# Optimization experiments

Measured on AMD Instinct MI355X. Metric: run time of the kernel, lower is better.

## Reference

```python
import jax, jax.numpy as jnp
import numpy as np

T, L, N, DR = 8, 8, 500, 32
D = 2 * DR          # dr2 = 64
K = 12              # neighbors per region
S = 2               # number_sp attention layers


def setup_inputs() -> dict:
    key = jax.random.key(0)
    ks = jax.random.split(key, 14)
    inp = {}
    inp["all_data_static"] = jax.random.normal(ks[0], (T, L, N, D), jnp.float32)
    inp["thre_nc"] = jax.random.uniform(ks[1], (T, L, N, 1), jnp.float32)
    inp["all_data_dynamic_now"] = jax.random.uniform(ks[2], (L, N, D), jnp.float32)
    inp["neigh_poi"] = jax.random.randint(ks[3], (N, K), 0, N)
    inp["neigh_road"] = jax.random.randint(ks[4], (N, K), 0, N)
    inp["neigh_record"] = jax.random.randint(ks[5], (N, K), 0, N)
    inp["w1"] = jax.random.normal(ks[6], (2 * D, D), jnp.float32) * 0.05
    inp["wq_all"] = jax.random.normal(ks[7], (2, 3, S, D, D), jnp.float32) * 0.05
    inp["wk_all"] = jax.random.normal(ks[8], (2, 3, S, D, D), jnp.float32) * 0.05
    inp["wd_all"] = jax.random.normal(ks[9], (2, 3, S, D, D), jnp.float32) * 0.05
    inp["wmix_all"] = jax.random.normal(ks[10], (2, 3, D), jnp.float32) * 0.1
    inp["conv_w"] = jax.random.normal(ks[11], (4, 2 * D + 1), jnp.float32) * 0.05
    inp["conv_b"] = jnp.zeros((4,), jnp.float32)
    inp["fin_w"] = jax.random.normal(ks[12], (N, N), jnp.float32) * 0.02
    inp["fin_b"] = jnp.ones((N,), jnp.float32)
    return inp


def _attention(data, neigh, wq, wk, wd):
    # data: (T,L,N,D), neigh: (N,K)
    dn = data[:, :, neigh, :]                                   # (T,L,N,K,D) gather
    q = jnp.einsum('tlnd,de->tlne', data, wq)                   # (T,L,N,D)
    k = jnp.einsum('tlnkd,de->tlnke', dn, wk)                   # (T,L,N,K,D)
    a = jax.nn.softmax(jnp.einsum('tlne,tlnke->tlnk', q, k), -1)
    out = q + jnp.einsum('tlnk,tlnke->tlne', a, k)              # residual on q
    return jax.nn.sigmoid(jnp.einsum('tlnd,de->tlne', out, wd))


def _multiattention(data, neighs, wq, wk, wd, wmix):
    outs = []
    for g in range(3):  # poi, road, record
        x = data
        for s in range(wq.shape[1]):
            x = _attention(x, neighs[g], wq[g, s], wk[g, s], wd[g, s])
        outs.append(x)
    return jax.nn.sigmoid(outs[0] * wmix[0] + outs[1] * wmix[1] + outs[2] * wmix[2])


def reference(all_data_static, thre_nc, all_data_dynamic_now,
              neigh_poi, neigh_road, neigh_record,
              w1, wq_all, wk_all, wd_all, wmix_all,
              conv_w, conv_b, fin_w, fin_b):
    # --- Evolution: gated recurrence over time steps 1..T-1 ---
    def evo_step(now, xs):
        st, th = xs  # (L,N,D), (L,N,1)
        new = jax.nn.sigmoid(jnp.concatenate([now, st], -1) @ w1 * th
                             + now * (1.0 - th))
        return new, (new, new - now)
    now_final, (dyn_rest, diffs) = jax.lax.scan(
        evo_step, all_data_dynamic_now, (all_data_static[1:], thre_nc[1:]))
    all_dyn = jnp.concatenate([all_data_dynamic_now[None], dyn_rest], 0)  # (T,L,N,D)

    neighs = (neigh_poi, neigh_road, neigh_record)
    dyn = _multiattention(all_dyn, neighs, wq_all[0], wk_all[0], wd_all[0], wmix_all[0])
    sta = _multiattention(all_data_static, neighs, wq_all[1], wk_all[1], wd_all[1], wmix_all[1])
    x = jnp.concatenate([dyn, sta], -1)                          # (T,L,N,2D)

    # --- ConvLSTM, kernel (1,1), hidden_dim=1 -> pointwise gated recurrence ---
    h0 = jnp.zeros((x.shape[0], x.shape[2], 1), x.dtype)         # (T,N,1)
    def cell(carry, xt):  # xt: (T,N,2D)
        h, c = carry
        gates = jnp.concatenate([xt, h], -1) @ conv_w.T + conv_b  # (T,N,4)
        i = jax.nn.sigmoid(gates[..., 0:1])
        f = jax.nn.sigmoid(gates[..., 1:2])
        o = jax.nn.sigmoid(gates[..., 2:3])
        g = jnp.tanh(gates[..., 3:4])
        c2 = f * c + i * g
        h2 = o * jnp.tanh(c2)
        return (h2, c2), None
    (h_last, _), _ = jax.lax.scan(cell, (h0, h0), jnp.swapaxes(x, 0, 1))

    out = jax.nn.sigmoid(h_last[..., 0] @ fin_w.T + fin_b)       # (T,N)
    return out, now_final, diffs
```

## Files before the change

### kernel.cpp

```cpp
#include <hip/hip_runtime.h>
#include <math.h>

namespace {
constexpr int kT = 8, kL = 8, kN = 500, kD = 64, kK = 12;
constexpr int kLN  = kL * kN;
constexpr int kTLN = kT * kL * kN;
constexpr int kBUF = kTLN * kD;
constexpr int XS = 68;
constexpr int EVR = 16;
}

__device__ __forceinline__ float sigf(float v) { return 1.f / (1.f + __expf(-v)); }

__device__ __forceinline__ float tanh_fast(float v) {
    float e = __expf(-2.f * fabsf(v));
    float t = (1.f - e) / (1.f + e);
    return copysignf(t, v);
}

__device__ __forceinline__ float row_allreduce16(float v) {
    v += __int_as_float(__builtin_amdgcn_update_dpp(
            0, __float_as_int(v), 0xB1, 0xf, 0xf, true));
    v += __int_as_float(__builtin_amdgcn_update_dpp(
            0, __float_as_int(v), 0x4E, 0xf, 0xf, true));
    v += __int_as_float(__builtin_amdgcn_update_dpp(
            0, __float_as_int(v), 0x124, 0xf, 0xf, true));
    v += __int_as_float(__builtin_amdgcn_update_dpp(
            0, __float_as_int(v), 0x128, 0xf, 0xf, true));
    return v;
}

__device__ __forceinline__ void stage_x(const float* __restrict__ src, float* lds,
                                        int row0, int M) {
    int r  = threadIdx.x >> 4;
    int c4 = (threadIdx.x & 15) << 2;
#pragma unroll
    for (int i = 0; i < 4; ++i) {
        int rr  = r + 16 * i;
        int row = row0 + rr;
        row = row < M ? row : M - 1;
        float4 v = *reinterpret_cast<const float4*>(src + (size_t)row * 64 + c4);
        *reinterpret_cast<float4*>(lds + rr * XS + c4) = v;
    }
}

template <int K>
__device__ __forceinline__ void stage_w(const float* __restrict__ w, float* lds) {
    const float4* s = reinterpret_cast<const float4*>(w);
    float4* d = reinterpret_cast<float4*>(lds);
#pragma unroll
    for (int i = 0; i < K / 16; ++i)
        d[threadIdx.x + 256 * i] = s[threadIdx.x + 256 * i];
}

__device__ __forceinline__ void gemm_core_gw(const float* ldsx,
                                             const float* __restrict__ gw,
                                             int rblk, int cblk, float4 acc[4]) {
#pragma unroll 4
    for (int k = 0; k < 64; k += 4) {
        float4 xv[4], wv[4];
#pragma unroll
        for (int i = 0; i < 4; ++i)
            xv[i] = *reinterpret_cast<const float4*>(ldsx + (4 * rblk + i) * XS + k);
#pragma unroll
        for (int d = 0; d < 4; ++d)
            wv[d] = *reinterpret_cast<const float4*>(gw + (k + d) * 64 + 4 * cblk);
#pragma unroll
        for (int i = 0; i < 4; ++i) {
            float xs[4] = {xv[i].x, xv[i].y, xv[i].z, xv[i].w};
#pragma unroll
            for (int d = 0; d < 4; ++d) {
                acc[i].x = fmaf(xs[d], wv[d].x, acc[i].x);
                acc[i].y = fmaf(xs[d], wv[d].y, acc[i].y);
                acc[i].z = fmaf(xs[d], wv[d].z, acc[i].z);
                acc[i].w = fmaf(xs[d], wv[d].w, acc[i].w);
            }
        }
    }
}

__device__ __forceinline__ void gemm_core2_bal(const float* ldsx, const float* ldswa,
                                               const float* __restrict__ gwb,
                                               int rblk, int cblk,
                                               float4 acca[4], float4 accb[4]) {
#pragma unroll 4
    for (int k = 0; k < 64; k += 4) {
        float4 xv[4], wa[4], wb[4];
#pragma unroll
        for (int i = 0; i < 4; ++i)
            xv[i] = *reinterpret_cast<const float4*>(ldsx + (4 * rblk + i) * XS + k);
#pragma unroll
        for (int d = 0; d < 4; ++d) {
            wa[d] = *reinterpret_cast<const float4*>(ldswa + (k + d) * 64 + 4 * cblk);
            wb[d] = *reinterpret_cast<const float4*>(gwb + (k + d) * 64 + 4 * cblk);
        }
#pragma unroll
        for (int i = 0; i < 4; ++i) {
            float xs[4] = {xv[i].x, xv[i].y, xv[i].z, xv[i].w};
#pragma unroll
            for (int d = 0; d < 4; ++d) {
                acca[i].x = fmaf(xs[d], wa[d].x, acca[i].x);
                acca[i].y = fmaf(xs[d], wa[d].y, acca[i].y);
                acca[i].z = fmaf(xs[d], wa[d].z, acca[i].z);
                acca[i].w = fmaf(xs[d], wa[d].w, acca[i].w);
                accb[i].x = fmaf(xs[d], wb[d].x, accb[i].x);
                accb[i].y = fmaf(xs[d], wb[d].y, accb[i].y);
                accb[i].z = fmaf(xs[d], wb[d].z, accb[i].z);
                accb[i].w = fmaf(xs[d], wb[d].w, accb[i].w);
            }
        }
    }
}

__global__ void __launch_bounds__(256) evo_all_kernel(const float* __restrict__ stat,
                                                      const float* __restrict__ thre,
                                                      const float* __restrict__ dyn0,
                                                      float* __restrict__ all_dyn,
                                                      float* __restrict__ diff,
                                                      float* __restrict__ now_final,
                                                      const float* __restrict__ w1) {
    __shared__ float ldsn[EVR * XS];
    __shared__ float ldss[EVR * XS];
    __shared__ float ldsw[128 * 64];
    int row0 = blockIdx.x * EVR;
    int r  = threadIdx.x >> 4;
    int c4 = (threadIdx.x & 15) << 2;
    *reinterpret_cast<float4*>(ldsn + r * XS + c4) =
        *reinterpret_cast<const float4*>(dyn0 + (size_t)(row0 + r) * 64 + c4);
    stage_w<128>(w1, ldsw);
    __syncthreads();
    {
        float4 x0 = *reinterpret_cast<const float4*>(ldsn + r * XS + c4);
        *reinterpret_cast<float4*>(all_dyn + (size_t)(row0 + r) * 64 + c4) = x0;
    }
#pragma unroll 1
    for (int t = 1; t < kT; ++t) {
        *reinterpret_cast<float4*>(ldss + r * XS + c4) =
            *reinterpret_cast<const float4*>(stat + (size_t)t * kLN * kD
                                             + (size_t)(row0 + r) * 64 + c4);
        __syncthreads();
        float4 acc = {0.f, 0.f, 0.f, 0.f};
#pragma unroll 4
        for (int k = 0; k < 64; k += 4) {
            float4 xv = *reinterpret_cast<const float4*>(ldsn + r * XS + k);
            float xs[4] = {xv.x, xv.y, xv.z, xv.w};
#pragma unroll
            for (int d = 0; d < 4; ++d) {
                float4 wv = *reinterpret_cast<const float4*>(ldsw + (k + d) * 64 + c4);
                acc.x = fmaf(xs[d], wv.x, acc.x);
                acc.y = fmaf(xs[d], wv.y, acc.y);
                acc.z = fmaf(xs[d], wv.z, acc.z);
                acc.w = fmaf(xs[d], wv.w, acc.w);
            }
        }
#pragma unroll 4
        for (int k = 0; k < 64; k += 4) {
            float4 xv = *reinterpret_cast<const float4*>(ldss + r * XS + k);
            float xs[4] = {xv.x, xv.y, xv.z, xv.w};
#pragma unroll
            for (int d = 0; d < 4; ++d) {
                float4 wv = *reinterpret_cast<const float4*>(ldsw + (64 + k + d) * 64 + c4);
                acc.x = fmaf(xs[d], wv.x, acc.x);
                acc.y = fmaf(xs[d], wv.y, acc.y);
                acc.z = fmaf(xs[d], wv.z, acc.z);
                acc.w = fmaf(xs[d], wv.w, acc.w);
            }
        }
        int row = row0 + r;
        float tt = thre[t * kLN + row];
        float4 xn = *reinterpret_cast<const float4*>(ldsn + r * XS + c4);
        float4 nv;
        nv.x = sigf(acc.x * tt + xn.x * (1.f - tt));
        nv.y = sigf(acc.y * tt + xn.y * (1.f - tt));
        nv.z = sigf(acc.z * tt + xn.z * (1.f - tt));
        nv.w = sigf(acc.w * tt + xn.w * (1.f - tt));
        float4 df;
        df.x = nv.x - xn.x; df.y = nv.y - xn.y;
        df.z = nv.z - xn.z; df.w = nv.w - xn.w;
        *reinterpret_cast<float4*>(all_dyn + ((size_t)t * kLN + row) * 64 + c4) = nv;
        *reinterpret_cast<float4*>(diff + ((size_t)(t - 1) * kLN + row) * 64 + c4) = df;
        if (t == kT - 1)
            *reinterpret_cast<float4*>(now_final + (size_t)row * 64 + c4) = nv;
        __syncthreads();
        *reinterpret_cast<float4*>(ldsn + r * XS + c4) = nv;
    }
}

__global__ void __launch_bounds__(256) gemm_qk(const float* __restrict__ Xdyn,
                                               const float* __restrict__ Xstat,
                                               const float* __restrict__ wq_all,
                                               const float* __restrict__ wk_all,
                                               float* __restrict__ b1,
                                               float* __restrict__ b2, int step) {
    __shared__ float ldsx[64 * XS];
    __shared__ float ldswq[64 * 64];
    int c = blockIdx.y;
    int m = c / 3;
    float* b1c = b1 + (size_t)c * kBUF;
    float* b2c = b2 + (size_t)c * kBUF;
    const float* X = step ? b1c : (m == 0 ? Xdyn : Xstat);
    size_t woff = (size_t)(c * 2 + step) * kD * kD;
    int row0 = blockIdx.x * 64;
    stage_x(X, ldsx, row0, kTLN);
    stage_w<64>(wq_all + woff, ldswq);
    __syncthreads();
    int rblk = threadIdx.x >> 4, cblk = threadIdx.x & 15;
    float4 aq[4] = {}, ak[4] = {};
    gemm_core2_bal(ldsx, ldswq, wk_all + woff, rblk, cblk, aq, ak);
#pragma unroll
    for (int i = 0; i < 4; ++i) {
        size_t row = row0 + 4 * rblk + i;
        *reinterpret_cast<float4*>(b1c + row * 64 + 4 * cblk) = aq[i];
        *reinterpret_cast<float4*>(b2c + row * 64 + 4 * cblk) = ak[i];
    }
}

__global__ void __launch_bounds__(256) scorewd_kernel(float* __restrict__ b1,
                                                      const float* __restrict__ b2,
                                                      const int* __restrict__ npoi,
                                                      const int* __restrict__ nroad,
                                                      const int* __restrict__ nrec,
                                                      const float* __restrict__ wd_all,
                                                      int step) {
    __shared__ float ldsx[64 * XS];
    int p   = blockIdx.y * gridDim.x + blockIdx.x;
    int xcd = p & 7;
    int gid = xcd * 375 + (p >> 3);
    int c    = gid / 500;
    int tile = gid - c * 500;
    int g = c % 3;
    float* b1c = b1 + (size_t)c * kBUF;
    const float* b2c = b2 + (size_t)c * kBUF;
    const int* neigh = (g == 0) ? npoi : (g == 1) ? nroad : nrec;
    const float* gw = wd_all + (size_t)(c * 2 + step) * kD * kD;

    int lane = threadIdx.x & 63;
    int wv   = threadIdx.x >> 6;
    int sub  = lane >> 4;
    int gq   = lane & 15;
    int row0 = tile * 64;
#pragma unroll 1
    for (int pp = 0; pp < 4; ++pp) {
        int lr  = pp * 16 + wv * 4 + sub;
        int row = row0 + lr;
        int n   = row % kN;
        int slab = row - n;
        float4 q = *(reinterpret_cast<const float4*>(b1c) + (size_t)row * 16 + gq);
        const int4* nbp = reinterpret_cast<const int4*>(neigh + n * kK);
        int4 nb0 = nbp[0], nb1 = nbp[1], nb2 = nbp[2];
        int nb[12] = {nb0.x, nb0.y, nb0.z, nb0.w, nb1.x, nb1.y, nb1.z, nb1.w,
                      nb2.x, nb2.y, nb2.z, nb2.w};
        float4 kv[12];
        float sc[12];
#pragma unroll
        for (int j = 0; j < 12; ++j) {
            kv[j] = *(reinterpret_cast<const float4*>(b2c) + (size_t)(slab + nb[j]) * 16 + gq);
            sc[j] = q.x * kv[j].x + q.y * kv[j].y + q.z * kv[j].z + q.w * kv[j].w;
        }
#pragma unroll
        for (int j = 0; j < 12; ++j) sc[j] = row_allreduce16(sc[j]);
        float mx = sc[0];
#pragma unroll
        for (int j = 1; j < 12; ++j) mx = fmaxf(mx, sc[j]);
        float ssum = 0.f;
#pragma unroll
        for (int j = 0; j < 12; ++j) { sc[j] = __expf(sc[j] - mx); ssum += sc[j]; }
        float inv = 1.f / ssum;
        float4 o = q;
#pragma unroll
        for (int j = 0; j < 12; ++j) {
            float a = sc[j] * inv;
            o.x = fmaf(a, kv[j].x, o.x);
            o.y = fmaf(a, kv[j].y, o.y);
            o.z = fmaf(a, kv[j].z, o.z);
            o.w = fmaf(a, kv[j].w, o.w);
        }
        *reinterpret_cast<float4*>(ldsx + lr * XS + 4 * gq) = o;
    }
    __syncthreads();
    int rblk = threadIdx.x >> 4, cblk = threadIdx.x & 15;
    float4 acc[4] = {};
    gemm_core_gw(ldsx, gw, rblk, cblk, acc);
#pragma unroll
    for (int i = 0; i < 4; ++i) {
        size_t idx = ((size_t)(row0 + 4 * rblk + i)) * 64 + 4 * cblk;
        float4 y;
        y.x = sigf(acc[i].x); y.y = sigf(acc[i].y);
        y.z = sigf(acc[i].z); y.w = sigf(acc[i].w);
        *reinterpret_cast<float4*>(b1c + idx) = y;
    }
}

__global__ void __launch_bounds__(256) lstm_kernel(const float* __restrict__ b1,
                                                   const float* __restrict__ wmix,
                                                   const float* __restrict__ cw,
                                                   const float* __restrict__ cb,
                                                   float* __restrict__ hlast) {
    int lane = threadIdx.x & 63;
    int wv   = threadIdx.x >> 6;
    int sub  = lane >> 4;
    int fq   = lane & 15;
    int cell = blockIdx.x * 16 + wv * 4 + sub;
    int t = cell / kN, n = cell % kN;
    float wd_[4][4], ws_[4][4], wh[4], bb[4];
#pragma unroll
    for (int gg = 0; gg < 4; ++gg) {
#pragma unroll
        for (int k = 0; k < 4; ++k) {
            wd_[gg][k] = cw[gg * 129 + fq * 4 + k];
            ws_[gg][k] = cw[gg * 129 + 64 + fq * 4 + k];
        }
        wh[gg] = cw[gg * 129 + 128];
        bb[gg] = cb[gg];
    }
    float4 wm[6];
#pragma unroll
    for (int j = 0; j < 6; ++j)
        wm[j] = *reinterpret_cast<const float4*>(wmix + j * 64 + fq * 4);
    float h = 0.f, cc = 0.f;
#pragma unroll 1
    for (int l = 0; l < kL; ++l) {
        size_t row16 = ((size_t)(t * kL + l) * kN + n) * 16 + fq;
        float4 y[6];
#pragma unroll
        for (int j = 0; j < 6; ++j)
            y[j] = *(reinterpret_cast<const float4*>(b1) + (size_t)j * (kBUF / 4) + row16);
        float4 xd, xs;
        xd.x = sigf(y[0].x * wm[0].x + y[1].x * wm[1].x + y[2].x * wm[2].x);
        xd.y = sigf(y[0].y * wm[0].y + y[1].y * wm[1].y + y[2].y * wm[2].y);
        xd.z = sigf(y[0].z * wm[0].z + y[1].z * wm[1].z + y[2].z * wm[2].z);
        xd.w = sigf(y[0].w * wm[0].w + y[1].w * wm[1].w + y[2].w * wm[2].w);
        xs.x = sigf(y[3].x * wm[3].x + y[4].x * wm[4].x + y[5].x * wm[5].x);
        xs.y = sigf(y[3].y * wm[3].y + y[4].y * wm[4].y + y[5].y * wm[5].y);
        xs.z = sigf(y[3].z * wm[3].z + y[4].z * wm[4].z + y[5].z * wm[5].z);
        xs.w = sigf(y[3].w * wm[3].w + y[4].w * wm[4].w + y[5].w * wm[5].w);
        float gsum[4];
#pragma unroll
        for (int gg = 0; gg < 4; ++gg) {
            float v = xd.x * wd_[gg][0] + xd.y * wd_[gg][1]
                    + xd.z * wd_[gg][2] + xd.w * wd_[gg][3];
            v += xs.x * ws_[gg][0] + xs.y * ws_[gg][1]
               + xs.z * ws_[gg][2] + xs.w * ws_[gg][3];
            gsum[gg] = v;
        }
#pragma unroll
        for (int gg = 0; gg < 4; ++gg) gsum[gg] = row_allreduce16(gsum[gg]);
        float gi = sigf(gsum[0] + bb[0] + h * wh[0]);
        float gf = sigf(gsum[1] + bb[1] + h * wh[1]);
        float go = sigf(gsum[2] + bb[2] + h * wh[2]);
        float gg_ = tanh_fast(gsum[3] + bb[3] + h * wh[3]);
        cc = gf * cc + gi * gg_;
        h = go * tanh_fast(cc);
    }
    if (fq == 0) hlast[cell] = h;
}

__global__ void final_kernel(const float* __restrict__ h, const float* __restrict__ fw,
                             const float* __restrict__ fb, float* __restrict__ out) {
    int wave = threadIdx.x >> 6, lane = threadIdx.x & 63;
    int o = blockIdx.x * 4 + wave;
    int t = o / kN, m = o % kN;
    float acc = 0.f;
    for (int n = lane; n < kN; n += 64)
        acc = fmaf(h[t * kN + n], fw[(size_t)m * kN + n], acc);
#pragma unroll
    for (int off = 32; off > 0; off >>= 1) acc += __shfl_xor(acc, off);
    if (lane == 0) out[o] = sigf(acc + fb[m]);
}

extern "C" void kernel_launch(void* const* d_in, const int* in_sizes, int n_in,
                              void* d_out, int out_size, void* d_ws, size_t ws_size,
                              hipStream_t stream) {
    const float* stat   = (const float*)d_in[0];
    const float* thre   = (const float*)d_in[1];
    const float* dyn0   = (const float*)d_in[2];
    const int*   npoi   = (const int*)d_in[3];
    const int*   nroad  = (const int*)d_in[4];
    const int*   nrec   = (const int*)d_in[5];
    const float* w1     = (const float*)d_in[6];
    const float* wq_all = (const float*)d_in[7];
    const float* wk_all = (const float*)d_in[8];
    const float* wd_all = (const float*)d_in[9];
    const float* wmix   = (const float*)d_in[10];
    const float* conv_w = (const float*)d_in[11];
    const float* conv_b = (const float*)d_in[12];
    const float* fin_w  = (const float*)d_in[13];
    const float* fin_b  = (const float*)d_in[14];

    float* out       = (float*)d_out;
    float* now_final = out + kT * kN;
    float* diffs     = now_final + (size_t)kLN * kD;

    float* ws      = (float*)d_ws;
    float* all_dyn = ws;
    float* b1      = ws + (size_t)kBUF;
    float* b2      = ws + 7 * (size_t)kBUF;
    float* hlast   = ws + 13 * (size_t)kBUF;

    evo_all_kernel<<<kLN / EVR, 256, 0, stream>>>(stat, thre, dyn0,
                                                  all_dyn, diffs, now_final, w1);

    dim3 agrid(kTLN / 64, 6);
    gemm_qk<<<agrid, 256, 0, stream>>>(all_dyn, stat, wq_all, wk_all, b1, b2, 0);
    scorewd_kernel<<<agrid, 256, 0, stream>>>(b1, b2, npoi, nroad, nrec, wd_all, 0);
    gemm_qk<<<agrid, 256, 0, stream>>>(all_dyn, stat, wq_all, wk_all, b1, b2, 1);
    scorewd_kernel<<<agrid, 256, 0, stream>>>(b1, b2, npoi, nroad, nrec, wd_all, 1);

    lstm_kernel<<<kT * kN / 16, 256, 0, stream>>>(b1, wmix, conv_w, conv_b, hlast);
    final_kernel<<<kT * kN / 4, 256, 0, stream>>>(hlast, fin_w, fin_b, out);
}
```

Before: 316.9 us.

## Fuse static-branch QK projection into evolution kernel launch to overlap work

The static-branch (c=3..5) first-step Q/K GEMM does not depend on the dynamic evolution recurrence, so its 1500 tiles are appended as extra blocks to the evolution kernel. The following gemm_qk launch now covers only the three dynamic channels. This lets the long, low-parallelism evolution recurrence (250 blocks) share the GPU with independent GEMM blocks and cuts one launch's worth of serialization. It also removes the row clamp in stage_x, since the row count divides evenly, and enlarges the fused kernel's shared memory to the union of both uses, which may lower occupancy.

After: 304.8 us. 1.04x faster.

```diff
diff --git a/kernel.cpp b/kernel.cpp
--- a/kernel.cpp
+++ b/kernel.cpp
@@ -31,15 +31,13 @@
 }
 
 __device__ __forceinline__ void stage_x(const float* __restrict__ src, float* lds,
-                                        int row0, int M) {
+                                        int row0) {
     int r  = threadIdx.x >> 4;
     int c4 = (threadIdx.x & 15) << 2;
 #pragma unroll
     for (int i = 0; i < 4; ++i) {
         int rr  = r + 16 * i;
-        int row = row0 + rr;
-        row = row < M ? row : M - 1;
-        float4 v = *reinterpret_cast<const float4*>(src + (size_t)row * 64 + c4);
+        float4 v = *reinterpret_cast<const float4*>(src + (size_t)(row0 + rr) * 64 + c4);
         *reinterpret_cast<float4*>(lds + rr * XS + c4) = v;
     }
 }
@@ -112,77 +110,109 @@
     }
 }
 
-__global__ void __launch_bounds__(256) evo_all_kernel(const float* __restrict__ stat,
-                                                      const float* __restrict__ thre,
-                                                      const float* __restrict__ dyn0,
-                                                      float* __restrict__ all_dyn,
-                                                      float* __restrict__ diff,
-                                                      float* __restrict__ now_final,
-                                                      const float* __restrict__ w1) {
-    __shared__ float ldsn[EVR * XS];
-    __shared__ float ldss[EVR * XS];
-    __shared__ float ldsw[128 * 64];
-    int row0 = blockIdx.x * EVR;
-    int r  = threadIdx.x >> 4;
-    int c4 = (threadIdx.x & 15) << 2;
-    *reinterpret_cast<float4*>(ldsn + r * XS + c4) =
-        *reinterpret_cast<const float4*>(dyn0 + (size_t)(row0 + r) * 64 + c4);
-    stage_w<128>(w1, ldsw);
+__device__ __forceinline__ void gemm_qk_body(const float* __restrict__ X,
+                                             const float* __restrict__ wq,
+                                             const float* __restrict__ wk,
+                                             float* __restrict__ b1c,
+                                             float* __restrict__ b2c,
+                                             int row0, float* ldsx, float* ldswq) {
+    stage_x(X, ldsx, row0);
+    stage_w<64>(wq, ldswq);
     __syncthreads();
-    {
-        float4 x0 = *reinterpret_cast<const float4*>(ldsn + r * XS + c4);
-        *reinterpret_cast<float4*>(all_dyn + (size_t)(row0 + r) * 64 + c4) = x0;
-    }
+    int rblk = threadIdx.x >> 4, cblk = threadIdx.x & 15;
+    float4 aq[4] = {}, ak[4] = {};
+    gemm_core2_bal(ldsx, ldswq, wk, rblk, cblk, aq, ak);
+#pragma unroll
+    for (int i = 0; i < 4; ++i) {
+        size_t row = row0 + 4 * rblk + i;
+        *reinterpret_cast<float4*>(b1c + row * 64 + 4 * cblk) = aq[i];
+        *reinterpret_cast<float4*>(b2c + row * 64 + 4 * cblk) = ak[i];
+    }
+}
+
+__global__ void __launch_bounds__(256) evo_statqk_kernel(
+        const float* __restrict__ stat, const float* __restrict__ thre,
+        const float* __restrict__ dyn0, float* __restrict__ all_dyn,
+        float* __restrict__ diff, float* __restrict__ now_final,
+        const float* __restrict__ w1, const float* __restrict__ wq_all,
+        const float* __restrict__ wk_all, float* __restrict__ b1,
+        float* __restrict__ b2) {
+    __shared__ float lds[2 * EVR * XS + 128 * 64];
+    if (blockIdx.x < kLN / EVR) {
+        float* ldsn = lds;
+        float* ldss = lds + EVR * XS;
+        float* ldsw = lds + 2 * EVR * XS;
+        int row0 = blockIdx.x * EVR;
+        int r  = threadIdx.x >> 4;
+        int c4 = (threadIdx.x & 15) << 2;
+        *reinterpret_cast<float4*>(ldsn + r * XS + c4) =
+            *reinterpret_cast<const float4*>(dyn0 + (size_t)(row0 + r) * 64 + c4);
+        stage_w<128>(w1, ldsw);
+        __syncthreads();
+        {
+            float4 x0 = *reinterpret_cast<const float4*>(ldsn + r * XS + c4);
+            *reinterpret_cast<float4*>(all_dyn + (size_t)(row0 + r) * 64 + c4) = x0;
+        }
 #pragma unroll 1
-    for (int t = 1; t < kT; ++t) {
-        *reinterpret_cast<float4*>(ldss + r * XS + c4) =
-            *reinterpret_cast<const float4*>(stat + (size_t)t * kLN * kD
-                                             + (size_t)(row0 + r) * 64 + c4);
-        __syncthreads();
-        float4 acc = {0.f, 0.f, 0.f, 0.f};
+        for (int t = 1; t < kT; ++t) {
+            *reinterpret_cast<float4*>(ldss + r * XS + c4) =
+                *reinterpret_cast<const float4*>(stat + (size_t)t * kLN * kD
+                                                 + (size_t)(row0 + r) * 64 + c4);
+            __syncthreads();
+            float4 acc = {0.f, 0.f, 0.f, 0.f};
 #pragma unroll 4
-        for (int k = 0; k < 64; k += 4) {
-            float4 xv = *reinterpret_cast<const float4*>(ldsn + r * XS + k);
-            float xs[4] = {xv.x, xv.y, xv.z, xv.w};
-#pragma unroll
-            for (int d = 0; d < 4; ++d) {
-                float4 wv = *reinterpret_cast<const float4*>(ldsw + (k + d) * 64 + c4);
-                acc.x = fmaf(xs[d], wv.x, acc.x);
-                acc.y = fmaf(xs[d], wv.y, acc.y);
-                acc.z = fmaf(xs[d], wv.z, acc.z);
-                acc.w = fmaf(xs[d], wv.w, acc.w);
+            for (int k = 0; k < 64; k += 4) {
+                float4 xv = *reinterpret_cast<const float4*>(ldsn + r * XS + k);
+                float xs[4] = {xv.x, xv.y, xv.z, xv.w};
+#pragma unroll
+                for (int d = 0; d < 4; ++d) {
+                    float4 wv = *reinterpret_cast<const float4*>(ldsw + (k + d) * 64 + c4);
+                    acc.x = fmaf(xs[d], wv.x, acc.x);
+                    acc.y = fmaf(xs[d], wv.y, acc.y);
+                    acc.z = fmaf(xs[d], wv.z, acc.z);
+                    acc.w = fmaf(xs[d], wv.w, acc.w);
+                }
             }
-        }
 #pragma unroll 4
-        for (int k = 0; k < 64; k += 4) {
-            float4 xv = *reinterpret_cast<const float4*>(ldss + r * XS + k);
-            float xs[4] = {xv.x, xv.y, xv.z, xv.w};
-#pragma unroll
-            for (int d = 0; d < 4; ++d) {
-                float4 wv = *reinterpret_cast<const float4*>(ldsw + (64 + k + d) * 64 + c4);
-                acc.x = fmaf(xs[d], wv.x, acc.x);
-                acc.y = fmaf(xs[d], wv.y, acc.y);
-                acc.z = fmaf(xs[d], wv.z, acc.z);
-                acc.w = fmaf(xs[d], wv.w, acc.w);
+            for (int k = 0; k < 64; k += 4) {
+                float4 xv = *reinterpret_cast<const float4*>(ldss + r * XS + k);
+                float xs[4] = {xv.x, xv.y, xv.z, xv.w};
+#pragma unroll
+                for (int d = 0; d < 4; ++d) {
+                    float4 wv = *reinterpret_cast<const float4*>(ldsw + (64 + k + d) * 64 + c4);
+                    acc.x = fmaf(xs[d], wv.x, acc.x);
+                    acc.y = fmaf(xs[d], wv.y, acc.y);
+                    acc.z = fmaf(xs[d], wv.z, acc.z);
+                    acc.w = fmaf(xs[d], wv.w, acc.w);
+                }
             }
-        }
-        int row = row0 + r;
-        float tt = thre[t * kLN + row];
-        float4 xn = *reinterpret_cast<const float4*>(ldsn + r * XS + c4);
-        float4 nv;
-        nv.x = sigf(acc.x * tt + xn.x * (1.f - tt));
-        nv.y = sigf(acc.y * tt + xn.y * (1.f - tt));
-        nv.z = sigf(acc.z * tt + xn.z * (1.f - tt));
-        nv.w = sigf(acc.w * tt + xn.w * (1.f - tt));
-        float4 df;
-        df.x = nv.x - xn.x; df.y = nv.y - xn.y;
-        df.z = nv.z - xn.z; df.w = nv.w - xn.w;
-        *reinterpret_cast<float4*>(all_dyn + ((size_t)t * kLN + row) * 64 + c4) = nv;
-        *reinterpret_cast<float4*>(diff + ((size_t)(t - 1) * kLN + row) * 64 + c4) = df;
-        if (t == kT - 1)
-            *reinterpret_cast<float4*>(now_final + (size_t)row * 64 + c4) = nv;
-        __syncthreads();
-        *reinterpret_cast<float4*>(ldsn + r * XS + c4) = nv;
+            int row = row0 + r;
+            float tt = thre[t * kLN + row];
+            float4 xn = *reinterpret_cast<const float4*>(ldsn + r * XS + c4);
+            float4 nv;
+            nv.x = sigf(acc.x * tt + xn.x * (1.f - tt));
+            nv.y = sigf(acc.y * tt + xn.y * (1.f - tt));
+            nv.z = sigf(acc.z * tt + xn.z * (1.f - tt));
+            nv.w = sigf(acc.w * tt + xn.w * (1.f - tt));
+            float4 df;
+            df.x = nv.x - xn.x; df.y = nv.y - xn.y;
+            df.z = nv.z - xn.z; df.w = nv.w - xn.w;
+            *reinterpret_cast<float4*>(all_dyn + ((size_t)t * kLN + row) * 64 + c4) = nv;
+            *reinterpret_cast<float4*>(diff + ((size_t)(t - 1) * kLN + row) * 64 + c4) = df;
+            if (t == kT - 1)
+                *reinterpret_cast<float4*>(now_final + (size_t)row * 64 + c4) = nv;
+            __syncthreads();
+            *reinterpret_cast<float4*>(ldsn + r * XS + c4) = nv;
+        }
+    } else {
+        int b = blockIdx.x - kLN / EVR;
+        int c = 3 + b / 500;
+        int tile = b - (c - 3) * 500;
+        float* b1c = b1 + (size_t)c * kBUF;
+        float* b2c = b2 + (size_t)c * kBUF;
+        size_t woff = (size_t)(c * 2) * kD * kD;
+        gemm_qk_body(stat, wq_all + woff, wk_all + woff, b1c, b2c,
+                     tile * 64, lds, lds + 64 * XS);
     }
 }
 
@@ -200,19 +230,8 @@
     float* b2c = b2 + (size_t)c * kBUF;
     const float* X = step ? b1c : (m == 0 ? Xdyn : Xstat);
     size_t woff = (size_t)(c * 2 + step) * kD * kD;
-    int row0 = blockIdx.x * 64;
-    stage_x(X, ldsx, row0, kTLN);
-    stage_w<64>(wq_all + woff, ldswq);
-    __syncthreads();
-    int rblk = threadIdx.x >> 4, cblk = threadIdx.x & 15;
-    float4 aq[4] = {}, ak[4] = {};
-    gemm_core2_bal(ldsx, ldswq, wk_all + woff, rblk, cblk, aq, ak);
-#pragma unroll
-    for (int i = 0; i < 4; ++i) {
-        size_t row = row0 + 4 * rblk + i;
-        *reinterpret_cast<float4*>(b1c + row * 64 + 4 * cblk) = aq[i];
-        *reinterpret_cast<float4*>(b2c + row * 64 + 4 * cblk) = ak[i];
-    }
+    gemm_qk_body(X, wq_all + woff, wk_all + woff, b1c, b2c,
+                 blockIdx.x * 64, ldsx, ldswq);
 }
 
 __global__ void __launch_bounds__(256) scorewd_kernel(float* __restrict__ b1,
@@ -397,11 +416,12 @@
     float* b2      = ws + 7 * (size_t)kBUF;
     float* hlast   = ws + 13 * (size_t)kBUF;
 
-    evo_all_kernel<<<kLN / EVR, 256, 0, stream>>>(stat, thre, dyn0,
-                                                  all_dyn, diffs, now_final, w1);
-
-    dim3 agrid(kTLN / 64, 6);
-    gemm_qk<<<agrid, 256, 0, stream>>>(all_dyn, stat, wq_all, wk_all, b1, b2, 0);
+    evo_statqk_kernel<<<kLN / EVR + 1500, 256, 0, stream>>>(
+        stat, thre, dyn0, all_dyn, diffs, now_final, w1, wq_all, wk_all, b1, b2);
+
+    dim3 dgrid(500, 3);
+    dim3 agrid(500, 6);
+    gemm_qk<<<dgrid, 256, 0, stream>>>(all_dyn, stat, wq_all, wk_all, b1, b2, 0);
     scorewd_kernel<<<agrid, 256, 0, stream>>>(b1, b2, npoi, nroad, nrec, wd_all, 0);
     gemm_qk<<<agrid, 256, 0, stream>>>(all_dyn, stat, wq_all, wk_all, b1, b2, 1);
     scorewd_kernel<<<agrid, 256, 0, stream>>>(b1, b2, npoi, nroad, nrec, wd_all, 1);
```
